# Kernel tuning notes

Hardware: AMD Instinct MI355X
Metric: run time of the kernel (lower is better)

Reference implementation:

```python
import jax, jax.numpy as jnp
import numpy as np

B = 32          # batch_size
S = 64          # num_subgraph
D = 8           # dim_multi_hot (module-level global in source repo)
NE = S * D      # num_edges = 512
NNODES = 1024
E = 150000      # incidence rows
IN_UNITS = [16, 32, 32]
OUT_UNITS = [32, 32, 16]


def _glorot(key, shape):
    # glorot_normal over last two dims (out, in)
    fan_out, fan_in = shape[-2], shape[-1]
    std = (2.0 / (fan_in + fan_out)) ** 0.5
    return std * jax.random.normal(key, shape, dtype=jnp.float32)


def setup_inputs() -> dict:
    key = jax.random.key(0)
    ks = jax.random.split(key, 10)
    nodes_features = jax.random.normal(ks[0], (NNODES * S, IN_UNITS[0]), dtype=jnp.float32)
    c0 = jax.random.randint(ks[1], (E,), 0, B, dtype=jnp.int32)
    c1 = jax.random.randint(ks[2], (E,), 0, NNODES, dtype=jnp.int32)
    c2 = jax.random.randint(ks[3], (E,), 0, S, dtype=jnp.int32)
    c3 = jax.random.randint(ks[4], (E,), 0, D, dtype=jnp.int32)
    incidence_matrix = jnp.stack([c0, c1, c2, c3], axis=1)
    return {
        'nodes_features': nodes_features,
        'in_core0': _glorot(ks[5], (NE, IN_UNITS[1], IN_UNITS[0])),
        'in_bias0': jnp.zeros((NE, IN_UNITS[1], 1), jnp.float32),
        'in_core1': _glorot(ks[6], (NE, IN_UNITS[2], IN_UNITS[1])),
        'in_bias1': jnp.zeros((NE, IN_UNITS[2], 1), jnp.float32),
        'out_core0': _glorot(ks[7], (NE, OUT_UNITS[1], OUT_UNITS[0])),
        'out_bias0': jnp.zeros((NE, OUT_UNITS[1], 1), jnp.float32),
        'out_core1': _glorot(ks[8], (NE, OUT_UNITS[2], OUT_UNITS[1])),
        'out_bias1': jnp.zeros((NE, OUT_UNITS[2], 1), jnp.float32),
        'incidence_matrix': incidence_matrix,
    }


def reference(nodes_features, in_core0, in_bias0, in_core1, in_bias1,
              out_core0, out_bias0, out_core1, out_bias1, incidence_matrix):
    c0 = incidence_matrix[:, 0]
    c1 = incidence_matrix[:, 1]
    c2 = incidence_matrix[:, 2]
    c3 = incidence_matrix[:, 3]

    # gather node features per incidence row: [E, in0]
    x = nodes_features[c1 * S + c2]
    eidx = c2 * D + c3  # per-edge weight index, < NE

    # per-edge MLP (gathered batched matmul + bias + relu)
    for W, b in ((in_core0, in_bias0), (in_core1, in_bias1)):
        x = jax.nn.relu(jnp.einsum('eoi,ei->eo', W[eidx], x) + b[eidx, :, 0])

    # unsorted segment mean over irregular edge groups
    seg = c0 * (D * S) + c2 * D + c3
    nseg = B * S * D
    sums = jax.ops.segment_sum(x, seg, num_segments=nseg)           # [B*NE, 32]
    cnt = jax.ops.segment_sum(jnp.ones((x.shape[0], 1), x.dtype), seg, num_segments=nseg)
    ef = jnp.where(cnt > 0, sums / jnp.maximum(cnt, 1.0), 0.0)       # [B*NE, 32]

    # output MLP: weights tiled over batch (einsum avoids explicit repeat)
    ef = ef.reshape(B, NE, -1)
    for W, b in ((out_core0, out_bias0), (out_core1, out_bias1)):
        ef = jax.nn.relu(jnp.einsum('eoi,bei->beo', W, ef) + b[None, :, :, 0])

    return ef.reshape(B * NE, OUT_UNITS[-1], 1)
```

## Files before the change

kernel.cpp:

```cpp
#include <hip/hip_runtime.h>

#define B_    32
#define S_    64
#define D_    8
#define NE_   512
#define E_    150000
#define CAP   448

#define SC_BLK   1024
#define SC_EPT   4
#define SC_EPB   (SC_BLK * SC_EPT)
#define SC_GRID  ((E_ + SC_EPB - 1) / SC_EPB)

#define GC_PITCH 32

typedef __attribute__((ext_vector_type(8)))  short  short8;
typedef __attribute__((ext_vector_type(16))) float  float16;

__device__ __forceinline__ unsigned short f2bf(float f) {
    union { float f; unsigned int u; } cv; cv.f = f;
    unsigned int u = cv.u;
    return (unsigned short)((u + 0x7fffu + ((u >> 16) & 1u)) >> 16);
}
__device__ __forceinline__ unsigned int pack2bf(float a, float b) {
    return (unsigned int)f2bf(a) | ((unsigned int)f2bf(b) << 16);
}

__global__ __launch_bounds__(SC_BLK)
void scatter_csr(const int* __restrict__ inc,
                 int* __restrict__ gcnt,
                 int* __restrict__ payload) {
    __shared__ int lcount[NE_];
    __shared__ int lbase[NE_];
    const int tid = threadIdx.x;

    if (tid < NE_) lcount[tid] = 0;
    __syncthreads();

    int ei[SC_EPT], lp[SC_EPT], pl[SC_EPT];
    #pragma unroll
    for (int i = 0; i < SC_EPT; ++i) {
        const int e = blockIdx.x * SC_EPB + i * SC_BLK + tid;
        ei[i] = -1;
        if (e < E_) {
            const int4 c = ((const int4*)inc)[e];
            ei[i] = c.z * D_ + c.w;
            pl[i] = (c.x << 16) | (c.y * S_ + c.z);
            lp[i] = atomicAdd(&lcount[ei[i]], 1);
        }
    }
    __syncthreads();

    if (tid < NE_) {
        const int c = lcount[tid];
        lbase[tid] = c ? atomicAdd(&gcnt[tid * GC_PITCH], c) : 0;
    }
    __syncthreads();

    #pragma unroll
    for (int i = 0; i < SC_EPT; ++i) {
        if (ei[i] >= 0) {
            const int s = lbase[ei[i]] + lp[i];
            if (s < CAP) payload[ei[i] * CAP + s] = pl[i];
        }
    }
}


#define TILE_COMPUTE(bXv, pvv, vldv)                                            \
  {                                                                             \
    float16 c0;                                                                 \
    _Pragma("unroll")                                                           \
    for (int r = 0; r < 16; ++r)                                                \
        c0[r] = bias0s[(r & 3) + 8 * (r >> 2) + 4 * q];                         \
    c0 = __builtin_amdgcn_mfma_f32_32x32x16_bf16(aWa, (bXv), c0, 0, 0, 0);      \
    unsigned Pw[8];                                                             \
    _Pragma("unroll")                                                           \
    for (int j = 0; j < 8; ++j)                                                 \
        Pw[j] = pack2bf(fmaxf(c0[2 * j], 0.f), fmaxf(c0[2 * j + 1], 0.f));      \
    asm("v_permlane32_swap_b32 %0, %1" : "+v"(Pw[0]), "+v"(Pw[2]));             \
    asm("v_permlane32_swap_b32 %0, %1" : "+v"(Pw[1]), "+v"(Pw[3]));             \
    asm("v_permlane32_swap_b32 %0, %1" : "+v"(Pw[4]), "+v"(Pw[6]));             \
    asm("v_permlane32_swap_b32 %0, %1" : "+v"(Pw[5]), "+v"(Pw[7]));             \
    union { unsigned u[4]; short8 s; } H0c, H1c;                                \
    H0c.u[0] = Pw[0]; H0c.u[1] = Pw[1]; H0c.u[2] = Pw[2]; H0c.u[3] = Pw[3];     \
    H1c.u[0] = Pw[4]; H1c.u[1] = Pw[5]; H1c.u[2] = Pw[6]; H1c.u[3] = Pw[7];     \
    float16 c1;                                                                 \
    _Pragma("unroll")                                                           \
    for (int r = 0; r < 16; ++r)                                                \
        c1[r] = bias1s[(r & 3) + 8 * (r >> 2) + 4 * q];                         \
    c1 = __builtin_amdgcn_mfma_f32_32x32x16_bf16(aWb0, H0c.s, c1, 0, 0, 0);     \
    c1 = __builtin_amdgcn_mfma_f32_32x32x16_bf16(aWb1, H1c.s, c1, 0, 0, 0);     \
    if (vldv) {                                                                 \
        const int b_e = ((pvv) >> 16) & 31;                                     \
        _Pragma("unroll")                                                       \
        for (int r = 0; r < 16; ++r)                                            \
            atomicAdd(&acc[b_e][(r & 3) + 8 * (r >> 2) + 4 * q],                \
                      fmaxf(c1[r], 0.f));                                       \
        if (q == 0) atomicAdd(&cnts[b_e], 1.f);                                 \
    }                                                                           \
  }

__global__ __launch_bounds__(512, 4)
void main_mfma(const float* __restrict__ nf,
               const float* __restrict__ iw0, const float* __restrict__ ib0,
               const float* __restrict__ iw1, const float* __restrict__ ib1,
               const float* __restrict__ ow0, const float* __restrict__ ob0,
               const float* __restrict__ ow1, const float* __restrict__ ob1,
               const int* __restrict__ gcnt, const int* __restrict__ payload,
               float* __restrict__ out) {
    const int bid  = blockIdx.x;
    const int tid  = threadIdx.x;
    const int lane = tid & 63;
    const int wav  = tid >> 6;
    const int e32  = lane & 31;
    const int q    = lane >> 5;

    __shared__ float acc[32][33];
    __shared__ float hb[32][33];
    __shared__ float cnts[32];
    __shared__ float q0t[32 * 33];
    __shared__ float q1t[32 * 17];
    __shared__ float qb0s[32], qb1s[16];
    __shared__ float bias0s[32], bias1s[32];

    const int n = min(gcnt[bid * GC_PITCH], CAP);

    const int s0 = (wav << 5) + e32;
    const int s1 = s0 + 256;
    const int pv0 = payload[bid * CAP + s0];
    const int pv1 = payload[bid * CAP + s1];

    short8 aWa, aWb0, aWb1;
    {
        const float* wa = iw0 + (size_t)bid * 512 + e32 * 16 + q * 8;
        float4 u0 = ((const float4*)wa)[0], u1 = ((const float4*)wa)[1];
        unsigned int p[4] = { pack2bf(u0.x,u0.y), pack2bf(u0.z,u0.w),
                              pack2bf(u1.x,u1.y), pack2bf(u1.z,u1.w) };
        aWa = *(short8*)p;
    }
    {
        const float* wb = iw1 + (size_t)bid * 1024 + e32 * 32 + q * 8;
        float4 u0 = ((const float4*)wb)[0], u1 = ((const float4*)wb)[1];
        unsigned int p[4] = { pack2bf(u0.x,u0.y), pack2bf(u0.z,u0.w),
                              pack2bf(u1.x,u1.y), pack2bf(u1.z,u1.w) };
        aWb0 = *(short8*)p;
        const float* wb2 = wb + 16;
        float4 u2 = ((const float4*)wb2)[0], u3 = ((const float4*)wb2)[1];
        unsigned int p2[4] = { pack2bf(u2.x,u2.y), pack2bf(u2.z,u2.w),
                               pack2bf(u3.x,u3.y), pack2bf(u3.z,u3.w) };
        aWb1 = *(short8*)p2;
    }

    const bool v0 = s0 < n;
    const bool v1 = s1 < n;
    short8 bX0, bX1;
    {
        const float4* xp = (const float4*)(nf + (size_t)(pv0 & 0xFFFF) * 16 + q * 8);
        float4 u0 = xp[0], u1 = xp[1];
        unsigned int pk[4] = { pack2bf(u0.x,u0.y), pack2bf(u0.z,u0.w),
                               pack2bf(u1.x,u1.y), pack2bf(u1.z,u1.w) };
        bX0 = *(short8*)pk;
    }
    {
        const float4* xp = (const float4*)(nf + (size_t)(pv1 & 0xFFFF) * 16 + q * 8);
        float4 u0 = xp[0], u1 = xp[1];
        unsigned int pk[4] = { pack2bf(u0.x,u0.y), pack2bf(u0.z,u0.w),
                               pack2bf(u1.x,u1.y), pack2bf(u1.z,u1.w) };
        bX1 = *(short8*)pk;
    }

    for (int i = tid; i < 1024; i += 512) {
        const int o = i >> 5, k = i & 31;
        q0t[k * 33 + o] = ow0[(size_t)bid * 1024 + i];
    }
    { const int o = tid >> 5, k = tid & 31;
      q1t[k * 17 + o] = ow1[(size_t)bid * 512 + tid]; }
    if (tid < 32)       { bias0s[tid] = ib0[bid * 32 + tid]; cnts[tid] = 0.f; }
    else if (tid < 64)  bias1s[tid - 32] = ib1[bid * 32 + (tid - 32)];
    else if (tid < 96)  qb0s[tid - 64] = ob0[bid * 32 + (tid - 64)];
    else if (tid < 112) qb1s[tid - 96] = ob1[bid * 16 + (tid - 96)];
    for (int i = tid; i < 32 * 33; i += 512) ((float*)acc)[i] = 0.f;
    __syncthreads();

    TILE_COMPUTE(bX0, pv0, v0);
    TILE_COMPUTE(bX1, pv1, v1);
    __syncthreads();

    {
        const int b  = tid >> 4;
        const int j  = tid & 15;
        const float cv  = cnts[b];
        const float inv = cv > 0.f ? 1.0f / cv : 0.0f;
        #pragma unroll
        for (int s = 0; s < 2; ++s) {
            const int oo = j * 2 + s;
            float d = 0.f;
            #pragma unroll
            for (int k = 0; k < 32; ++k) d = fmaf(q0t[k * 33 + oo], acc[b][k], d);
            hb[b][oo] = fmaxf(fmaf(d, inv, qb0s[oo]), 0.f);
        }
    }
    __syncthreads();

    {
        const int b = tid >> 4;
        const int o = tid & 15;
        float d = qb1s[o];
        #pragma unroll
        for (int k = 0; k < 32; ++k) d = fmaf(q1t[k * 17 + o], hb[b][k], d);
        out[((size_t)b * NE_ + bid) * 16 + o] = fmaxf(d, 0.f);
    }
}

extern "C" void kernel_launch(void* const* d_in, const int* in_sizes, int n_in,
                              void* d_out, int out_size, void* d_ws, size_t ws_size,
                              hipStream_t stream) {
    const float* nf  = (const float*)d_in[0];
    const float* iw0 = (const float*)d_in[1];
    const float* ib0 = (const float*)d_in[2];
    const float* iw1 = (const float*)d_in[3];
    const float* ib1 = (const float*)d_in[4];
    const float* ow0 = (const float*)d_in[5];
    const float* ob0 = (const float*)d_in[6];
    const float* ow1 = (const float*)d_in[7];
    const float* ob1 = (const float*)d_in[8];
    const int*   inc = (const int*)d_in[9];

    int* gcnt    = (int*)d_ws;
    int* payload = (int*)((char*)d_ws + NE_ * GC_PITCH * 4);

    hipMemsetAsync(gcnt, 0, NE_ * GC_PITCH * sizeof(int), stream);
    scatter_csr<<<SC_GRID, SC_BLK, 0, stream>>>(inc, gcnt, payload);
    main_mfma<<<NE_, 512, 0, stream>>>(nf, iw0, ib0, iw1, ib1, ow0, ob0, ow1, ob1,
                                       gcnt, payload, (float*)d_out);
}
```

Before: 119.4 us.

## Fuse CSR scatter into main kernel with per-block incidence scan over four edges

Replaces the memset, the global CSR scatter kernel and the per-edge MFMA kernel with a single kernel. Each of 128 blocks handles four edge-weight indices. It scans the entire incidence matrix, collects matching rows into a shared-memory list, then runs the per-edge MLP, segment mean and output MLP for each of its four edges. This removes two launches and the global atomics and workspace traffic. In exchange, every block re-reads all 150k incidence rows, which adds a lot of redundant L2 traffic. Only 128 blocks are launched, so occupancy is lower.

After: 200.0 us. +67.6%, slower.

```diff
diff --git a/kernel.cpp b/kernel.cpp
--- a/kernel.cpp
+++ b/kernel.cpp
@@ -6,13 +6,9 @@
 #define NE_   512
 #define E_    150000
 #define CAP   448
-
-#define SC_BLK   1024
-#define SC_EPT   4
-#define SC_EPB   (SC_BLK * SC_EPT)
-#define SC_GRID  ((E_ + SC_EPB - 1) / SC_EPB)
-
-#define GC_PITCH 32
+#define NB    4
+#define GRID  (NE_ / NB)
+#define BLK   1024
 
 typedef __attribute__((ext_vector_type(8)))  short  short8;
 typedef __attribute__((ext_vector_type(16))) float  float16;
@@ -25,55 +21,21 @@
 __device__ __forceinline__ unsigned int pack2bf(float a, float b) {
     return (unsigned int)f2bf(a) | ((unsigned int)f2bf(b) << 16);
 }
-
-__global__ __launch_bounds__(SC_BLK)
-void scatter_csr(const int* __restrict__ inc,
-                 int* __restrict__ gcnt,
-                 int* __restrict__ payload) {
-    __shared__ int lcount[NE_];
-    __shared__ int lbase[NE_];
-    const int tid = threadIdx.x;
-
-    if (tid < NE_) lcount[tid] = 0;
-    __syncthreads();
-
-    int ei[SC_EPT], lp[SC_EPT], pl[SC_EPT];
-    #pragma unroll
-    for (int i = 0; i < SC_EPT; ++i) {
-        const int e = blockIdx.x * SC_EPB + i * SC_BLK + tid;
-        ei[i] = -1;
-        if (e < E_) {
-            const int4 c = ((const int4*)inc)[e];
-            ei[i] = c.z * D_ + c.w;
-            pl[i] = (c.x << 16) | (c.y * S_ + c.z);
-            lp[i] = atomicAdd(&lcount[ei[i]], 1);
-        }
-    }
-    __syncthreads();
-
-    if (tid < NE_) {
-        const int c = lcount[tid];
-        lbase[tid] = c ? atomicAdd(&gcnt[tid * GC_PITCH], c) : 0;
-    }
-    __syncthreads();
-
-    #pragma unroll
-    for (int i = 0; i < SC_EPT; ++i) {
-        if (ei[i] >= 0) {
-            const int s = lbase[ei[i]] + lp[i];
-            if (s < CAP) payload[ei[i] * CAP + s] = pl[i];
-        }
-    }
-}
-
-
-#define TILE_COMPUTE(bXv, pvv, vldv)                                            \
+__device__ __forceinline__ short8 load_pack16(const float* p) {
+    float4 u0 = ((const float4*)p)[0], u1 = ((const float4*)p)[1];
+    unsigned int pk[4] = { pack2bf(u0.x,u0.y), pack2bf(u0.z,u0.w),
+                           pack2bf(u1.x,u1.y), pack2bf(u1.z,u1.w) };
+    return *(short8*)pk;
+}
+
+
+#define TILE_COMPUTE(bb, bXv, pvv, vldv)                                        \
   {                                                                             \
     float16 c0;                                                                 \
     _Pragma("unroll")                                                           \
     for (int r = 0; r < 16; ++r)                                                \
-        c0[r] = bias0s[(r & 3) + 8 * (r >> 2) + 4 * q];                         \
-    c0 = __builtin_amdgcn_mfma_f32_32x32x16_bf16(aWa, (bXv), c0, 0, 0, 0);      \
+        c0[r] = bias0s[bb][(r & 3) + 8 * (r >> 2) + 4 * q];                     \
+    c0 = __builtin_amdgcn_mfma_f32_32x32x16_bf16(aWa[bb], (bXv), c0, 0, 0, 0);  \
     unsigned Pw[8];                                                             \
     _Pragma("unroll")                                                           \
     for (int j = 0; j < 8; ++j)                                                 \
@@ -88,26 +50,26 @@
     float16 c1;                                                                 \
     _Pragma("unroll")                                                           \
     for (int r = 0; r < 16; ++r)                                                \
-        c1[r] = bias1s[(r & 3) + 8 * (r >> 2) + 4 * q];                         \
-    c1 = __builtin_amdgcn_mfma_f32_32x32x16_bf16(aWb0, H0c.s, c1, 0, 0, 0);     \
-    c1 = __builtin_amdgcn_mfma_f32_32x32x16_bf16(aWb1, H1c.s, c1, 0, 0, 0);     \
+        c1[r] = bias1s[bb][(r & 3) + 8 * (r >> 2) + 4 * q];                     \
+    c1 = __builtin_amdgcn_mfma_f32_32x32x16_bf16(aWb0[bb], H0c.s, c1, 0, 0, 0); \
+    c1 = __builtin_amdgcn_mfma_f32_32x32x16_bf16(aWb1[bb], H1c.s, c1, 0, 0, 0); \
     if (vldv) {                                                                 \
         const int b_e = ((pvv) >> 16) & 31;                                     \
         _Pragma("unroll")                                                       \
         for (int r = 0; r < 16; ++r)                                            \
-            atomicAdd(&acc[b_e][(r & 3) + 8 * (r >> 2) + 4 * q],                \
+            atomicAdd(&acc[bb][b_e][(r & 3) + 8 * (r >> 2) + 4 * q],            \
                       fmaxf(c1[r], 0.f));                                       \
-        if (q == 0) atomicAdd(&cnts[b_e], 1.f);                                 \
+        if (q == 0) atomicAdd(&cnts[bb][b_e], 1.f);                             \
     }                                                                           \
   }
 
-__global__ __launch_bounds__(512, 4)
-void main_mfma(const float* __restrict__ nf,
+__global__ __launch_bounds__(BLK)
+void fused_all(const float* __restrict__ nf,
                const float* __restrict__ iw0, const float* __restrict__ ib0,
                const float* __restrict__ iw1, const float* __restrict__ ib1,
                const float* __restrict__ ow0, const float* __restrict__ ob0,
                const float* __restrict__ ow1, const float* __restrict__ ob1,
-               const int* __restrict__ gcnt, const int* __restrict__ payload,
+               const int* __restrict__ inc,
                float* __restrict__ out) {
     const int bid  = blockIdx.x;
     const int tid  = threadIdx.x;
@@ -115,101 +77,107 @@
     const int wav  = tid >> 6;
     const int e32  = lane & 31;
     const int q    = lane >> 5;
-
-    __shared__ float acc[32][33];
+    const int base = bid * NB;
+
+    __shared__ int   lcount[NB];
+    __shared__ int   elist[NB][CAP];
+    __shared__ float acc[NB][32][33];
+    __shared__ float cnts[NB][32];
     __shared__ float hb[32][33];
-    __shared__ float cnts[32];
-    __shared__ float q0t[32 * 33];
-    __shared__ float q1t[32 * 17];
-    __shared__ float qb0s[32], qb1s[16];
-    __shared__ float bias0s[32], bias1s[32];
-
-    const int n = min(gcnt[bid * GC_PITCH], CAP);
-
-    const int s0 = (wav << 5) + e32;
-    const int s1 = s0 + 256;
-    const int pv0 = payload[bid * CAP + s0];
-    const int pv1 = payload[bid * CAP + s1];
-
-    short8 aWa, aWb0, aWb1;
-    {
-        const float* wa = iw0 + (size_t)bid * 512 + e32 * 16 + q * 8;
-        float4 u0 = ((const float4*)wa)[0], u1 = ((const float4*)wa)[1];
-        unsigned int p[4] = { pack2bf(u0.x,u0.y), pack2bf(u0.z,u0.w),
-                              pack2bf(u1.x,u1.y), pack2bf(u1.z,u1.w) };
-        aWa = *(short8*)p;
-    }
-    {
-        const float* wb = iw1 + (size_t)bid * 1024 + e32 * 32 + q * 8;
-        float4 u0 = ((const float4*)wb)[0], u1 = ((const float4*)wb)[1];
-        unsigned int p[4] = { pack2bf(u0.x,u0.y), pack2bf(u0.z,u0.w),
-                              pack2bf(u1.x,u1.y), pack2bf(u1.z,u1.w) };
-        aWb0 = *(short8*)p;
-        const float* wb2 = wb + 16;
-        float4 u2 = ((const float4*)wb2)[0], u3 = ((const float4*)wb2)[1];
-        unsigned int p2[4] = { pack2bf(u2.x,u2.y), pack2bf(u2.z,u2.w),
-                               pack2bf(u3.x,u3.y), pack2bf(u3.z,u3.w) };
-        aWb1 = *(short8*)p2;
-    }
-
-    const bool v0 = s0 < n;
-    const bool v1 = s1 < n;
-    short8 bX0, bX1;
-    {
-        const float4* xp = (const float4*)(nf + (size_t)(pv0 & 0xFFFF) * 16 + q * 8);
-        float4 u0 = xp[0], u1 = xp[1];
-        unsigned int pk[4] = { pack2bf(u0.x,u0.y), pack2bf(u0.z,u0.w),
-                               pack2bf(u1.x,u1.y), pack2bf(u1.z,u1.w) };
-        bX0 = *(short8*)pk;
-    }
-    {
-        const float4* xp = (const float4*)(nf + (size_t)(pv1 & 0xFFFF) * 16 + q * 8);
-        float4 u0 = xp[0], u1 = xp[1];
-        unsigned int pk[4] = { pack2bf(u0.x,u0.y), pack2bf(u0.z,u0.w),
-                               pack2bf(u1.x,u1.y), pack2bf(u1.z,u1.w) };
-        bX1 = *(short8*)pk;
-    }
-
-    for (int i = tid; i < 1024; i += 512) {
-        const int o = i >> 5, k = i & 31;
-        q0t[k * 33 + o] = ow0[(size_t)bid * 1024 + i];
-    }
-    { const int o = tid >> 5, k = tid & 31;
-      q1t[k * 17 + o] = ow1[(size_t)bid * 512 + tid]; }
-    if (tid < 32)       { bias0s[tid] = ib0[bid * 32 + tid]; cnts[tid] = 0.f; }
-    else if (tid < 64)  bias1s[tid - 32] = ib1[bid * 32 + (tid - 32)];
-    else if (tid < 96)  qb0s[tid - 64] = ob0[bid * 32 + (tid - 64)];
-    else if (tid < 112) qb1s[tid - 96] = ob1[bid * 16 + (tid - 96)];
-    for (int i = tid; i < 32 * 33; i += 512) ((float*)acc)[i] = 0.f;
+    __shared__ float q0t[NB][32 * 33];
+    __shared__ float q1t[NB][32 * 17];
+    __shared__ float qb0s[NB][32], qb1s[NB][16];
+    __shared__ float bias0s[NB][32], bias1s[NB][32];
+
+    if (tid < NB) lcount[tid] = 0;
+
+    short8 aWa[NB], aWb0[NB], aWb1[NB];
+    #pragma unroll
+    for (int b = 0; b < NB; ++b) {
+        const int eidx = base + b;
+        aWa[b]  = load_pack16(iw0 + (size_t)eidx * 512  + e32 * 16 + q * 8);
+        aWb0[b] = load_pack16(iw1 + (size_t)eidx * 1024 + e32 * 32 + q * 8);
+        aWb1[b] = load_pack16(iw1 + (size_t)eidx * 1024 + e32 * 32 + 16 + q * 8);
+    }
+
+    #pragma unroll
+    for (int i0 = 0; i0 < 4; ++i0) {
+        const int i = i0 * BLK + tid;
+        const int b = i >> 10, idx = i & 1023;
+        const int o = idx >> 5, k = idx & 31;
+        q0t[b][k * 33 + o] = ow0[(size_t)(base + b) * 1024 + idx];
+    }
+    #pragma unroll
+    for (int i0 = 0; i0 < 2; ++i0) {
+        const int i = i0 * BLK + tid;
+        const int b = i >> 9, idx = i & 511;
+        const int o = idx >> 5, k = idx & 31;
+        q1t[b][k * 17 + o] = ow1[(size_t)(base + b) * 512 + idx];
+    }
+    if (tid < 128)      { bias0s[tid >> 5][tid & 31] = ib0[(base + (tid >> 5)) * 32 + (tid & 31)]; }
+    else if (tid < 256) { const int t = tid - 128; bias1s[t >> 5][t & 31] = ib1[(base + (t >> 5)) * 32 + (t & 31)]; }
+    else if (tid < 384) { const int t = tid - 256; qb0s[t >> 5][t & 31] = ob0[(base + (t >> 5)) * 32 + (t & 31)]; }
+    else if (tid < 448) { const int t = tid - 384; qb1s[t >> 4][t & 15] = ob1[(base + (t >> 4)) * 16 + (t & 15)]; }
+    else if (tid < 576) { const int t = tid - 448; ((float*)cnts)[t] = 0.f; }
+    for (int i = tid; i < NB * 32 * 33; i += BLK) ((float*)acc)[i] = 0.f;
     __syncthreads();
 
-    TILE_COMPUTE(bX0, pv0, v0);
-    TILE_COMPUTE(bX1, pv1, v1);
+    const int4* inc4 = (const int4*)inc;
+    #pragma unroll 2
+    for (int i = tid; i < E_; i += BLK) {
+        const int4 c = inc4[i];
+        const int lb = c.z * D_ + c.w - base;
+        if ((unsigned)lb < NB) {
+            const int slot = atomicAdd(&lcount[lb], 1);
+            if (slot < CAP) elist[lb][slot] = (c.x << 16) | (c.y * S_ + c.z);
+        }
+    }
     __syncthreads();
 
-    {
-        const int b  = tid >> 4;
+    int n_[NB], nt_[NB], pv_[NB]; bool v_[NB]; short8 bX_[NB];
+    const int s = (wav << 5) + e32;
+    #pragma unroll
+    for (int b = 0; b < NB; ++b) {
+        n_[b]  = min(lcount[b], CAP);
+        nt_[b] = (n_[b] + 31) >> 5;
+        v_[b]  = s < n_[b];
+        const int cs = n_[b] > 0 ? min(s, n_[b] - 1) : 0;
+        pv_[b] = elist[b][cs];
+    }
+    #pragma unroll
+    for (int b = 0; b < NB; ++b)
+        bX_[b] = load_pack16(nf + (size_t)(pv_[b] & 0xFFFF) * 16 + q * 8);
+
+    #pragma unroll
+    for (int b = 0; b < NB; ++b) {
+        if (wav < nt_[b]) {
+            TILE_COMPUTE(b, bX_[b], pv_[b], v_[b]);
+        }
+    }
+    __syncthreads();
+
+    if (tid < 512) {
+        const int b2 = tid >> 4;
         const int j  = tid & 15;
-        const float cv  = cnts[b];
-        const float inv = cv > 0.f ? 1.0f / cv : 0.0f;
         #pragma unroll
-        for (int s = 0; s < 2; ++s) {
-            const int oo = j * 2 + s;
-            float d = 0.f;
+        for (int b = 0; b < NB; ++b) {
+            const float cv  = cnts[b][b2];
+            const float inv = cv > 0.f ? 1.0f / cv : 0.0f;
             #pragma unroll
-            for (int k = 0; k < 32; ++k) d = fmaf(q0t[k * 33 + oo], acc[b][k], d);
-            hb[b][oo] = fmaxf(fmaf(d, inv, qb0s[oo]), 0.f);
+            for (int ss = 0; ss < 2; ++ss) {
+                const int oo = j * 2 + ss;
+                float d = 0.f;
+                #pragma unroll
+                for (int k = 0; k < 32; ++k)
+                    d = fmaf(q0t[b][k * 33 + oo], acc[b][b2][k], d);
+                hb[b2][oo] = fmaxf(fmaf(d, inv, qb0s[b][oo]), 0.f);
+            }
+            float d1 = qb1s[b][j];
+            #pragma unroll
+            for (int k = 0; k < 32; ++k)
+                d1 = fmaf(q1t[b][k * 17 + j], hb[b2][k], d1);
+            out[((size_t)b2 * NE_ + (base + b)) * 16 + j] = fmaxf(d1, 0.f);
         }
-    }
-    __syncthreads();
-
-    {
-        const int b = tid >> 4;
-        const int o = tid & 15;
-        float d = qb1s[o];
-        #pragma unroll
-        for (int k = 0; k < 32; ++k) d = fmaf(q1t[k * 17 + o], hb[b][k], d);
-        out[((size_t)b * NE_ + bid) * 16 + o] = fmaxf(d, 0.f);
     }
 }
 
@@ -227,11 +195,8 @@
     const float* ob1 = (const float*)d_in[8];
     const int*   inc = (const int*)d_in[9];
 
-    int* gcnt    = (int*)d_ws;
-    int* payload = (int*)((char*)d_ws + NE_ * GC_PITCH * 4);
-
-    hipMemsetAsync(gcnt, 0, NE_ * GC_PITCH * sizeof(int), stream);
-    scatter_csr<<<SC_GRID, SC_BLK, 0, stream>>>(inc, gcnt, payload);
-    main_mfma<<<NE_, 512, 0, stream>>>(nf, iw0, ib0, iw1, ib1, ow0, ob0, ow1, ob1,
-                                       gcnt, payload, (float*)d_out);
-}
+    (void)d_ws; (void)ws_size;
+
+    fused_all<<<GRID, BLK, 0, stream>>>(nf, iw0, ib0, iw1, ib1, ow0, ob0, ow1, ob1,
+                                        inc, (float*)d_out);
+}
```

## Replace global atomic CSR binning with per-block bins compacted in main kernel

Applied to the files above, without the earlier changes.

The scatter kernel no longer uses global atomics or a memset. Each block writes its edges into a fixed 32-slot bin per edge type, plus a per-block count. The main kernel then prefix-sums those counts with wave shuffles and compacts the payload into a shared-memory edge list before gathering features. This removes the memset launch and contended global atomics, at the cost of extra payload reads and an extra barrier in the main kernel. It also relies on no block having more than 32 rows for one edge type.

Measured after the change: 119.0 us. Within noise of the previous version (-0.3%).

```diff
diff --git a/kernel.cpp b/kernel.cpp
--- a/kernel.cpp
+++ b/kernel.cpp
@@ -11,8 +11,10 @@
 #define SC_EPT   4
 #define SC_EPB   (SC_BLK * SC_EPT)
 #define SC_GRID  ((E_ + SC_EPB - 1) / SC_EPB)
-
-#define GC_PITCH 32
+#define SLOTS    32
+#define PITCH    (SC_GRID * SLOTS)
+
+#define PAYLOAD_BYTE_OFF 131072
 
 typedef __attribute__((ext_vector_type(8)))  short  short8;
 typedef __attribute__((ext_vector_type(16))) float  float16;
@@ -27,11 +29,10 @@
 }
 
 __global__ __launch_bounds__(SC_BLK)
-void scatter_csr(const int* __restrict__ inc,
-                 int* __restrict__ gcnt,
-                 int* __restrict__ payload) {
+void scatter_bin(const int* __restrict__ inc,
+                 int* __restrict__ cnt2D,
+                 int* __restrict__ payload2D) {
     __shared__ int lcount[NE_];
-    __shared__ int lbase[NE_];
     const int tid = threadIdx.x;
 
     if (tid < NE_) lcount[tid] = 0;
@@ -49,21 +50,13 @@
             lp[i] = atomicAdd(&lcount[ei[i]], 1);
         }
     }
-    __syncthreads();
-
-    if (tid < NE_) {
-        const int c = lcount[tid];
-        lbase[tid] = c ? atomicAdd(&gcnt[tid * GC_PITCH], c) : 0;
-    }
-    __syncthreads();
-
     #pragma unroll
-    for (int i = 0; i < SC_EPT; ++i) {
-        if (ei[i] >= 0) {
-            const int s = lbase[ei[i]] + lp[i];
-            if (s < CAP) payload[ei[i] * CAP + s] = pl[i];
-        }
-    }
+    for (int i = 0; i < SC_EPT; ++i)
+        if (ei[i] >= 0 && lp[i] < SLOTS)
+            payload2D[ei[i] * PITCH + blockIdx.x * SLOTS + lp[i]] = pl[i];
+    __syncthreads();
+    if (tid < NE_)
+        cnt2D[tid * SC_GRID + blockIdx.x] = min(lcount[tid], SLOTS);
 }
 
 
@@ -107,12 +100,12 @@
                const float* __restrict__ iw1, const float* __restrict__ ib1,
                const float* __restrict__ ow0, const float* __restrict__ ob0,
                const float* __restrict__ ow1, const float* __restrict__ ob1,
-               const int* __restrict__ gcnt, const int* __restrict__ payload,
+               const int* __restrict__ cnt2D, const int* __restrict__ payload2D,
                float* __restrict__ out) {
     const int bid  = blockIdx.x;
     const int tid  = threadIdx.x;
+    const int wav  = tid >> 6;
     const int lane = tid & 63;
-    const int wav  = tid >> 6;
     const int e32  = lane & 31;
     const int q    = lane >> 5;
 
@@ -123,13 +116,28 @@
     __shared__ float q1t[32 * 17];
     __shared__ float qb0s[32], qb1s[16];
     __shared__ float bias0s[32], bias1s[32];
-
-    const int n = min(gcnt[bid * GC_PITCH], CAP);
-
-    const int s0 = (wav << 5) + e32;
-    const int s1 = s0 + 256;
-    const int pv0 = payload[bid * CAP + s0];
-    const int pv1 = payload[bid * CAP + s1];
+    __shared__ int   sbase[64], scount[64];
+    __shared__ int   sn;
+    __shared__ int   elist[512];
+
+    const int* Pb = payload2D + (size_t)bid * PITCH;
+    const int p0 = tid, p1 = tid + 512, p2 = tid + 1024;
+    const int r0 = Pb[p0];
+    const int r1 = Pb[p1];
+    const int r2 = (p2 < PITCH) ? Pb[p2] : 0;
+
+    if (tid < 64) {
+        int v = (tid < SC_GRID) ? cnt2D[bid * SC_GRID + tid] : 0;
+        scount[tid] = v;
+        int incl = v;
+        #pragma unroll
+        for (int off = 1; off < 64; off <<= 1) {
+            const int t = __shfl_up(incl, off);
+            if (tid >= off) incl += t;
+        }
+        sbase[tid] = incl - v;
+        if (tid == SC_GRID - 1) sn = min(incl, CAP);
+    }
 
     short8 aWa, aWb0, aWb1;
     {
@@ -147,27 +155,9 @@
         aWb0 = *(short8*)p;
         const float* wb2 = wb + 16;
         float4 u2 = ((const float4*)wb2)[0], u3 = ((const float4*)wb2)[1];
-        unsigned int p2[4] = { pack2bf(u2.x,u2.y), pack2bf(u2.z,u2.w),
-                               pack2bf(u3.x,u3.y), pack2bf(u3.z,u3.w) };
-        aWb1 = *(short8*)p2;
-    }
-
-    const bool v0 = s0 < n;
-    const bool v1 = s1 < n;
-    short8 bX0, bX1;
-    {
-        const float4* xp = (const float4*)(nf + (size_t)(pv0 & 0xFFFF) * 16 + q * 8);
-        float4 u0 = xp[0], u1 = xp[1];
-        unsigned int pk[4] = { pack2bf(u0.x,u0.y), pack2bf(u0.z,u0.w),
-                               pack2bf(u1.x,u1.y), pack2bf(u1.z,u1.w) };
-        bX0 = *(short8*)pk;
-    }
-    {
-        const float4* xp = (const float4*)(nf + (size_t)(pv1 & 0xFFFF) * 16 + q * 8);
-        float4 u0 = xp[0], u1 = xp[1];
-        unsigned int pk[4] = { pack2bf(u0.x,u0.y), pack2bf(u0.z,u0.w),
-                               pack2bf(u1.x,u1.y), pack2bf(u1.z,u1.w) };
-        bX1 = *(short8*)pk;
+        unsigned int p2k[4] = { pack2bf(u2.x,u2.y), pack2bf(u2.z,u2.w),
+                                pack2bf(u3.x,u3.y), pack2bf(u3.z,u3.w) };
+        aWb1 = *(short8*)p2k;
     }
 
     for (int i = tid; i < 1024; i += 512) {
@@ -182,6 +172,51 @@
     else if (tid < 112) qb1s[tid - 96] = ob1[bid * 16 + (tid - 96)];
     for (int i = tid; i < 32 * 33; i += 512) ((float*)acc)[i] = 0.f;
     __syncthreads();
+
+    {
+        const int blk0 = p0 >> 5, sl0 = p0 & 31;
+        if (sl0 < scount[blk0]) {
+            const int idx = sbase[blk0] + sl0;
+            if (idx < CAP) elist[idx] = r0;
+        }
+        const int blk1 = p1 >> 5, sl1 = p1 & 31;
+        if (sl1 < scount[blk1]) {
+            const int idx = sbase[blk1] + sl1;
+            if (idx < CAP) elist[idx] = r1;
+        }
+        if (p2 < PITCH) {
+            const int blk2 = p2 >> 5, sl2 = p2 & 31;
+            if (sl2 < scount[blk2]) {
+                const int idx = sbase[blk2] + sl2;
+                if (idx < CAP) elist[idx] = r2;
+            }
+        }
+    }
+    __syncthreads();
+
+    const int n  = sn;
+    const int s0 = (wav << 5) + e32;
+    const int s1 = s0 + 256;
+    const int pv0 = elist[s0];
+    const int pv1 = elist[s1];
+    const bool v0 = s0 < n;
+    const bool v1 = s1 < n;
+
+    short8 bX0, bX1;
+    {
+        const float4* xp = (const float4*)(nf + (size_t)(pv0 & 0xFFFF) * 16 + q * 8);
+        float4 u0 = xp[0], u1 = xp[1];
+        unsigned int pk[4] = { pack2bf(u0.x,u0.y), pack2bf(u0.z,u0.w),
+                               pack2bf(u1.x,u1.y), pack2bf(u1.z,u1.w) };
+        bX0 = *(short8*)pk;
+    }
+    {
+        const float4* xp = (const float4*)(nf + (size_t)(pv1 & 0xFFFF) * 16 + q * 8);
+        float4 u0 = xp[0], u1 = xp[1];
+        unsigned int pk[4] = { pack2bf(u0.x,u0.y), pack2bf(u0.z,u0.w),
+                               pack2bf(u1.x,u1.y), pack2bf(u1.z,u1.w) };
+        bX1 = *(short8*)pk;
+    }
 
     TILE_COMPUTE(bX0, pv0, v0);
     TILE_COMPUTE(bX1, pv1, v1);
@@ -227,11 +262,10 @@
     const float* ob1 = (const float*)d_in[8];
     const int*   inc = (const int*)d_in[9];
 
-    int* gcnt    = (int*)d_ws;
-    int* payload = (int*)((char*)d_ws + NE_ * GC_PITCH * 4);
-
-    hipMemsetAsync(gcnt, 0, NE_ * GC_PITCH * sizeof(int), stream);
-    scatter_csr<<<SC_GRID, SC_BLK, 0, stream>>>(inc, gcnt, payload);
+    int* cnt2D     = (int*)d_ws;
+    int* payload2D = (int*)((char*)d_ws + PAYLOAD_BYTE_OFF);
+
+    scatter_bin<<<SC_GRID, SC_BLK, 0, stream>>>(inc, cnt2D, payload2D);
     main_mfma<<<NE_, 512, 0, stream>>>(nf, iw0, ib0, iw1, ib1, ow0, ob0, ow1, ob1,
-                                       gcnt, payload, (float*)d_out);
-}
+                                       cnt2D, payload2D, (float*)d_out);
+}
```
